# Kernel tuning notes

Hardware: AMD Instinct MI355X
Metric: run time of the kernel (lower is better)

## Reference

```python
import jax, jax.numpy as jnp
import numpy as np

N_EMBD = 1024
N_HEADS = 16
HEAD_EMBD = N_EMBD // N_HEADS  # 64
TOTAL = N_HEADS * HEAD_EMBD


def setup_inputs() -> dict:
    key = jax.random.key(0)
    k_x, k_wqkv, k_bqkv, k_wo, k_bo = jax.random.split(key, 5)
    B, S = 2, 2048
    x = jax.random.normal(k_x, (B, S, N_EMBD), dtype=jnp.float32)
    # torch nn.Linear: weight (out, in), y = x @ W.T + b
    lim_qkv = 1.0 / np.sqrt(N_EMBD)
    W_qkv = jax.random.uniform(k_wqkv, (3 * TOTAL, N_EMBD), minval=-lim_qkv, maxval=lim_qkv, dtype=jnp.float32)
    b_qkv = jax.random.uniform(k_bqkv, (3 * TOTAL,), minval=-lim_qkv, maxval=lim_qkv, dtype=jnp.float32)
    lim_o = 1.0 / np.sqrt(TOTAL)
    W_out = jax.random.uniform(k_wo, (N_EMBD, TOTAL), minval=-lim_o, maxval=lim_o, dtype=jnp.float32)
    b_out = jax.random.uniform(k_bo, (N_EMBD,), minval=-lim_o, maxval=lim_o, dtype=jnp.float32)
    return {"x": x, "W_qkv": W_qkv, "b_qkv": b_qkv, "W_out": W_out, "b_out": b_out}


def reference(x, W_qkv, b_qkv, W_out, b_out):
    B, S, _ = x.shape
    qkv = x @ W_qkv.T + b_qkv  # (B, S, 3*H*E)
    # rearrange 'b s (t h e) -> t b h s e'
    qkv = qkv.reshape(B, S, 3, N_HEADS, HEAD_EMBD)
    q = jnp.transpose(qkv[:, :, 0], (0, 2, 1, 3))  # (B, H, S, E)
    k = jnp.transpose(qkv[:, :, 1], (0, 2, 1, 3))
    v = jnp.transpose(qkv[:, :, 2], (0, 2, 1, 3))
    scores = jnp.einsum('bhse,bhte->bhst', q, k) / jnp.sqrt(jnp.float32(HEAD_EMBD))
    # original: tril(scores) + triu(-10000, k=1) == strict-upper entries exactly -10000
    row = jnp.arange(S)[:, None]
    col = jnp.arange(S)[None, :]
    masked = jnp.where(col > row, jnp.float32(-10000.0), scores)
    attn = jax.nn.softmax(masked, axis=-1)  # (B, H, S, S)
    z = jnp.einsum('bhrc,bhce->bhre', attn, v)  # (B, H, S, E)
    z = jnp.transpose(z, (0, 2, 1, 3)).reshape(B, S, TOTAL)
    out = z @ W_out.T + b_out
    return (out, attn)
```

## Files before the change

### kernel.cpp

```cpp
#include <hip/hip_runtime.h>
#include <stdint.h>

typedef __attribute__((ext_vector_type(4))) float f32x4;
typedef __attribute__((ext_vector_type(8))) short short8v;
typedef __attribute__((ext_vector_type(4))) unsigned short ushort4v;

#define DEV __device__ __forceinline__
#define EXP2 __builtin_amdgcn_exp2f
#define WAITVM0 asm volatile("s_waitcnt vmcnt(0)" ::: "memory")
#define WAITVM2 asm volatile("s_waitcnt vmcnt(2)" ::: "memory")
#define WAITVM4 asm volatile("s_waitcnt vmcnt(4)" ::: "memory")
#define FENCE   asm volatile("" ::: "memory")
#define BARRIER __builtin_amdgcn_s_barrier()

DEV unsigned short f2bf(float x) {
    union { float f; uint32_t u; } v; v.f = x;
    uint32_t r = v.u + 0x7fffu + ((v.u >> 16) & 1u);
    return (unsigned short)(r >> 16);
}
DEV float bf2f(unsigned short h) {
    union { uint32_t u; float f; } v; v.u = ((uint32_t)h) << 16;
    return v.f;
}
DEV uint32_t cvtpk(float lo, float hi) {
    uint32_t r;
    asm("v_cvt_pk_bf16_f32 %0, %1, %2" : "=v"(r) : "v"(lo), "v"(hi));
    return r;
}
DEV f32x4 mfma16(short8v a, short8v b, f32x4 c) {
    return __builtin_amdgcn_mfma_f32_16x16x32_bf16(a, b, c, 0, 0, 0);
}
DEV void gload16(const unsigned short* g, unsigned short* l) {
    __builtin_amdgcn_global_load_lds(
        (const __attribute__((address_space(1))) unsigned int*)g,
        (__attribute__((address_space(3))) unsigned int*)l, 16, 0, 0);
}
DEV void ntstore4(float* p, f32x4 v) { __builtin_nontemporal_store(v, (f32x4*)p); }

__global__ void k_cvt3(const float* __restrict__ a, unsigned short* __restrict__ oa, int na4,
                       const float* __restrict__ b, unsigned short* __restrict__ ob, int nb4,
                       const float* __restrict__ c, unsigned short* __restrict__ oc, int nc4) {
    int i = blockIdx.x * blockDim.x + threadIdx.x;
    const float* in; unsigned short* out; int idx;
    if (i < na4) { in = a; out = oa; idx = i; }
    else if (i < na4 + nb4) { in = b; out = ob; idx = i - na4; }
    else { idx = i - na4 - nb4; if (idx >= nc4) return; in = c; out = oc; }
    f32x4 v = *(const f32x4*)(in + (size_t)idx * 4);
    ushort4v h;
#pragma unroll
    for (int j = 0; j < 4; ++j) h[j] = f2bf(v[j]);
    *(ushort4v*)(out + (size_t)idx * 4) = h;
}

template <int KDIM>
DEV void gemm_core(const unsigned short* __restrict__ APTR,
                   const unsigned short* __restrict__ BPTR,
                   f32x4 (&acc)[4][4]) {
    __shared__ __align__(16) unsigned short As[2][128 * 32], Bs[2][128 * 32];
    int tid = threadIdx.x, lane = tid & 63, w = tid >> 6;
    int bm = blockIdx.x, bn = blockIdx.y;
    int wr = (w >> 1) * 64, wc = (w & 1) * 64;
    int lrow = lane & 15, lseg = lane >> 4;
#pragma unroll
    for (int m = 0; m < 4; ++m)
#pragma unroll
        for (int n = 0; n < 4; ++n) acc[m][n] = (f32x4){0.f, 0.f, 0.f, 0.f};
    auto STAGE = [&](int buf, int k0) {
#pragma unroll
        for (int i = 0; i < 2; ++i) {
            int ch = i * 256 + tid;
            int row = ch >> 2, seg = ch & 3;
            gload16(APTR + (size_t)(bm * 128 + row) * KDIM + k0 + seg * 8,
                    &As[buf][(i * 256 + (tid & ~63)) * 8]);
            gload16(BPTR + (size_t)(bn * 128 + row) * KDIM + k0 + seg * 8,
                    &Bs[buf][(i * 256 + (tid & ~63)) * 8]);
        }
    };
    const int NT = KDIM / 32;
    STAGE(0, 0);
    for (int t = 0; t < NT; ++t) {
        if (t < NT - 1) { STAGE((t + 1) & 1, (t + 1) * 32); WAITVM4; } else WAITVM0;
        BARRIER;
        const unsigned short* as = As[t & 1];
        const unsigned short* bs = Bs[t & 1];
        short8v fa[4], fb[4];
#pragma unroll
        for (int m = 0; m < 4; ++m) {
            fa[m] = *(const short8v*)(as + (wr + m * 16 + lrow) * 32 + lseg * 8);
            fb[m] = *(const short8v*)(bs + (wc + m * 16 + lrow) * 32 + lseg * 8);
        }
#pragma unroll
        for (int m = 0; m < 4; ++m)
#pragma unroll
            for (int n = 0; n < 4; ++n)
                acc[m][n] = mfma16(fa[m], fb[n], acc[m][n]);
        FENCE; BARRIER;
    }
}

__global__ __launch_bounds__(256) void k_gemm_qkv(
    const unsigned short* __restrict__ XB, const unsigned short* __restrict__ WB,
    const float* __restrict__ BIAS, unsigned short* __restrict__ QKVB) {
    f32x4 acc[4][4];
    gemm_core<1024>(XB, WB, acc);
    int tid = threadIdx.x, lane = tid & 63, w = tid >> 6;
    int bm = blockIdx.x, bn = blockIdx.y;
    int wr = (w >> 1) * 64, wc = (w & 1) * 64;
    int lrow = lane & 15, lseg = lane >> 4;
    const int N = 3072;
#pragma unroll
    for (int n = 0; n < 4; ++n) {
        int col = bn * 128 + wc + n * 16 + lrow;
        float bv = BIAS[col];
#pragma unroll
        for (int m = 0; m < 4; ++m) {
            int row = bm * 128 + wr + m * 16 + lseg * 4;
#pragma unroll
            for (int i = 0; i < 4; ++i)
                QKVB[(size_t)(row + i) * N + col] = f2bf(acc[m][n][i] + bv);
        }
    }
}

__global__ __launch_bounds__(256) void k_gemm_out(
    const unsigned short* __restrict__ ZB, const unsigned short* __restrict__ WOB,
    const float* __restrict__ BIAS, float* __restrict__ OUT) {
    f32x4 acc[4][4];
    gemm_core<1024>(ZB, WOB, acc);
    int tid = threadIdx.x, lane = tid & 63, w = tid >> 6;
    int bm = blockIdx.x, bn = blockIdx.y;
    int wr = (w >> 1) * 64, wc = (w & 1) * 64;
    int lrow = lane & 15, lseg = lane >> 4;
    const int N = 1024;
#pragma unroll
    for (int n = 0; n < 4; ++n) {
        int col = bn * 128 + wc + n * 16 + lrow;
        float bv = BIAS[col];
#pragma unroll
        for (int m = 0; m < 4; ++m) {
            int row = bm * 128 + wr + m * 16 + lseg * 4;
#pragma unroll
            for (int i = 0; i < 4; ++i)
                OUT[(size_t)(row + i) * N + col] = acc[m][n][i] + bv;
        }
    }
}

__global__ void k_prep_v(const unsigned short* __restrict__ QKVB, unsigned short* __restrict__ VT) {
    __shared__ unsigned short vt[32][72];
    int bh = blockIdx.y, b = bh >> 4, h = bh & 15;
    int c0 = blockIdx.x * 32;
    int t = threadIdx.x;
    int c = t >> 3, e8 = (t & 7) * 8;
    *(short8v*)&vt[c][e8] =
        *(const short8v*)(QKVB + (size_t)(b * 2048 + c0 + c) * 3072 + 2048 + h * 64 + e8);
    __syncthreads();
    int e = t & 63, cg = t >> 6;
    unsigned short tmp[8];
#pragma unroll
    for (int i = 0; i < 8; ++i) tmp[i] = vt[cg * 8 + i][e];
    *(short8v*)(VT + ((size_t)bh * 64 + e) * 2048 + c0 + cg * 8) = *(short8v*)tmp;
}

__global__ __launch_bounds__(512) void k_attn(
    const unsigned short* __restrict__ QKVB, const unsigned short* __restrict__ VT,
    float* __restrict__ ATTN, unsigned short* __restrict__ Z) {
    __shared__ __align__(16) unsigned short KV[2][8192];
    __shared__ __align__(16) float Pl[8][16][68];

    const float SCALE = 0.18033688011112042f;
    int blk = blockIdx.x;
    int bh = blk & 31;
    int rtp = blk >> 5;
    int rt = (rtp < 8) ? (15 - rtp) : (rtp - 8);
    int b = bh >> 4, h = bh & 15;
    int tid = threadIdx.x, lane = tid & 63, w = tid >> 6;
    int lrow = lane & 15, lseg = lane >> 4;
    int r0 = rt * 128 + w * 16;
    int T = 2 * rt + 2;
    int Tw = (r0 >> 6) + 1;

    short8v qf[2];
    {
        const unsigned short* qp =
            QKVB + (size_t)(b * 2048 + r0 + lrow) * 3072 + h * 64 + lseg * 8;
#pragma unroll
        for (int kc = 0; kc < 2; ++kc) {
            short8v qr = *(const short8v*)(qp + kc * 32);
            short8v qs;
#pragma unroll
            for (int j = 0; j < 8; ++j)
                qs[j] = (short)f2bf(bf2f((unsigned short)qr[j]) * SCALE);
            qf[kc] = qs;
        }
    }

    auto STAGEKA = [&](int buf, int t) {
        const size_t kbase = ((size_t)b * 2048 + (size_t)t * 128) * 3072 + 1024 + h * 64;
#pragma unroll
        for (int i2 = 0; i2 < 2; ++i2) {
            int ch = i2 * 512 + tid;
            int c = ch >> 3, u = ch & 7, us = u ^ (c & 7);
            gload16(QKVB + kbase + (size_t)c * 3072 + us * 8,
                    &KV[buf][(i2 * 512 + (tid & ~63)) * 8]);
        }
    };
    float ls4[4] = {0.f, 0.f, 0.f, 0.f};
    int TA = rt + 1;
    STAGEKA(0, 0);
    for (int t = 0; t < TA; ++t) {
        if (t < TA - 1) { STAGEKA((t + 1) & 1, t + 1); WAITVM2; } else WAITVM0;
        BARRIER;
        const unsigned short* kb = KV[t & 1];
        f32x4 sc[8];
#pragma unroll
        for (int g = 0; g < 8; ++g) sc[g] = (f32x4){0.f, 0.f, 0.f, 0.f};
#pragma unroll
        for (int kc = 0; kc < 2; ++kc) {
            int uoff = (((kc * 4 + lseg) ^ (lrow & 7)) << 3);
#pragma unroll
            for (int g = 0; g < 8; ++g) {
                short8v kf = *(const short8v*)(kb + (g * 16 + lrow) * 64 + uoff);
                sc[g] = mfma16(qf[kc], kf, sc[g]);
            }
        }
        if (t < TA - 1) {
#pragma unroll
            for (int g = 0; g < 8; ++g)
#pragma unroll
                for (int i = 0; i < 4; ++i) ls4[i] += EXP2(sc[g][i]);
        } else {
            int c0 = t * 128;
#pragma unroll
            for (int g = 0; g < 8; ++g)
#pragma unroll
                for (int i = 0; i < 4; ++i) {
                    float sv = (c0 + g * 16 + lrow > r0 + lseg * 4 + i) ? -1e30f : sc[g][i];
                    ls4[i] += EXP2(sv);
                }
        }
        FENCE; BARRIER;
    }
#pragma unroll
    for (int off = 1; off < 16; off <<= 1)
#pragma unroll
        for (int i = 0; i < 4; ++i) ls4[i] += __shfl_xor(ls4[i], off, 64);
    float invl[4];
#pragma unroll
    for (int i = 0; i < 4; ++i) invl[i] = 1.0f / ls4[i];

    auto STAGEKB = [&](int buf, int t) {
        const size_t kbase = ((size_t)b * 2048 + (size_t)t * 64) * 3072 + 1024 + h * 64;
        int c = tid >> 3, u = tid & 7, us = u ^ (c & 7);
        gload16(QKVB + kbase + (size_t)c * 3072 + us * 8, &KV[buf][(tid & ~63) * 8]);
    };
    auto STAGEVB = [&](int buf, int t) {
        const size_t vbase = (size_t)bh * 64 * 2048 + (size_t)t * 64;
        int e = tid >> 3, u = tid & 7, us = u ^ (e & 7);
        gload16(VT + vbase + (size_t)e * 2048 + us * 8, &KV[buf][4096 + (tid & ~63) * 8]);
    };

    float* ab = ATTN + ((size_t)bh * 2048 + r0) * 2048;
    f32x4 zacc[4];
#pragma unroll
    for (int i = 0; i < 4; ++i) zacc[i] = (f32x4){0.f, 0.f, 0.f, 0.f};

    STAGEKB(0, 0); STAGEVB(0, 0);
    for (int t = 0; t < T; ++t) {
        if (t < T - 1) { STAGEKB((t + 1) & 1, t + 1); STAGEVB((t + 1) & 1, t + 1); WAITVM2; }
        else WAITVM0;
        BARRIER;
        if (t < Tw) {
            const unsigned short* kb = KV[t & 1];
            const unsigned short* vb = KV[t & 1] + 4096;
            int c0 = t * 64;
            f32x4 sc[4];
#pragma unroll
            for (int g = 0; g < 4; ++g) sc[g] = (f32x4){0.f, 0.f, 0.f, 0.f};
#pragma unroll
            for (int kc = 0; kc < 2; ++kc) {
                int uoff = (((kc * 4 + lseg) ^ (lrow & 7)) << 3);
#pragma unroll
                for (int g = 0; g < 4; ++g) {
                    short8v kf = *(const short8v*)(kb + (g * 16 + lrow) * 64 + uoff);
                    sc[g] = mfma16(qf[kc], kf, sc[g]);
                }
            }
            if (t < Tw - 1) {
#pragma unroll
                for (int g = 0; g < 4; ++g)
#pragma unroll
                    for (int i = 0; i < 4; ++i)
                        Pl[w][lseg * 4 + i][g * 16 + lrow] = EXP2(sc[g][i]) * invl[i];
            } else {
#pragma unroll
                for (int g = 0; g < 4; ++g)
#pragma unroll
                    for (int i = 0; i < 4; ++i) {
                        float sv = (c0 + g * 16 + lrow > r0 + lseg * 4 + i) ? -1e30f : sc[g][i];
                        Pl[w][lseg * 4 + i][g * 16 + lrow] = EXP2(sv) * invl[i];
                    }
            }
            short8v pf[2];
#pragma unroll
            for (int kc = 0; kc < 2; ++kc) {
                f32x4 p0 = *(const f32x4*)&Pl[w][lrow][kc * 32 + lseg * 8];
                f32x4 p1 = *(const f32x4*)&Pl[w][lrow][kc * 32 + lseg * 8 + 4];
                union { uint32_t u[4]; short8v s; } pu;
                pu.u[0] = cvtpk(p0[0], p0[1]);
                pu.u[1] = cvtpk(p0[2], p0[3]);
                pu.u[2] = cvtpk(p1[0], p1[1]);
                pu.u[3] = cvtpk(p1[2], p1[3]);
                pf[kc] = pu.s;
            }
#pragma unroll
            for (int kc = 0; kc < 2; ++kc) {
                int uoff = (((kc * 4 + lseg) ^ (lrow & 7)) << 3);
#pragma unroll
                for (int et = 0; et < 4; ++et) {
                    short8v vf = *(const short8v*)(vb + (et * 16 + lrow) * 64 + uoff);
                    zacc[et] = mfma16(pf[kc], vf, zacc[et]);
                }
            }
            {
                int row4 = lane >> 4, cq = lane & 15;
#pragma unroll
                for (int r4 = 0; r4 < 4; ++r4) {
                    int row = r4 * 4 + row4;
                    ntstore4(ab + (size_t)row * 2048 + c0 + cq * 4,
                             *(const f32x4*)(&Pl[w][row][cq * 4]));
                }
            }
        }
        FENCE; BARRIER;
    }

#pragma unroll
    for (int et = 0; et < 4; ++et)
#pragma unroll
        for (int i = 0; i < 4; ++i)
            Z[(size_t)(b * 2048 + r0 + lseg * 4 + i) * 1024 + h * 64 + et * 16 + lrow] =
                f2bf(zacc[et][i]);

    int czw = Tw * 64;
    const f32x4 zz = (f32x4){0.f, 0.f, 0.f, 0.f};
    for (int r = 0; r < 16; ++r) {
        float* rp = ab + (size_t)r * 2048;
        for (int c = czw + (lane << 2); c < 2048; c += 256)
            ntstore4(rp + c, zz);
    }
}

extern "C" void kernel_launch(void* const* d_in, const int* in_sizes, int n_in,
                              void* d_out, int out_size, void* d_ws, size_t ws_size,
                              hipStream_t stream) {
    const float* X    = (const float*)d_in[0];
    const float* Wqkv = (const float*)d_in[1];
    const float* Bqkv = (const float*)d_in[2];
    const float* Wout = (const float*)d_in[3];
    const float* Bout = (const float*)d_in[4];
    float* out  = (float*)d_out;
    float* attn = out + (size_t)4096 * 1024;

    char* ws = (char*)d_ws;
    unsigned short* QKVB = (unsigned short*)ws; ws += (size_t)4096 * 3072 * 2;
    unsigned short* VTp  = (unsigned short*)ws; ws += (size_t)32 * 64 * 2048 * 2;
    unsigned short* ZBp  = (unsigned short*)ws; ws += (size_t)4096 * 1024 * 2;
    unsigned short* XBp  = (unsigned short*)ws; ws += (size_t)4096 * 1024 * 2;
    unsigned short* WQBp = (unsigned short*)ws; ws += (size_t)3072 * 1024 * 2;
    unsigned short* WOBp = (unsigned short*)ws; ws += (size_t)1024 * 1024 * 2;

    const int na4 = 4096 * 1024 / 4, nb4 = 3072 * 1024 / 4, nc4 = 1024 * 1024 / 4;
    k_cvt3<<<(na4 + nb4 + nc4 + 255) / 256, 256, 0, stream>>>(
        X, XBp, na4, Wqkv, WQBp, nb4, Wout, WOBp, nc4);
    k_gemm_qkv<<<dim3(32, 24), 256, 0, stream>>>(XBp, WQBp, Bqkv, QKVB);
    k_prep_v<<<dim3(64, 32), 256, 0, stream>>>(QKVB, VTp);
    k_attn<<<512, 512, 0, stream>>>(QKVB, VTp, attn, ZBp);
    k_gemm_out<<<dim3(32, 8), 256, 0, stream>>>(ZBp, WOBp, Bout, out);
}
```

Baseline: 230.1 us.

## Split attention into row-sum kernel and PV kernel, move zero-fill earlier

Splits the attention kernel in two. The first kernel computes the softmax row sums, writes their inverses to a workspace buffer, and zero-fills the masked upper triangle of the attention matrix. The second kernel reads the inverse sums and does the probability write-out and PV accumulation. This shortens each kernel's critical path and shifts the zero-fill stores off the PV kernel. It costs an extra launch and an extra Rinv buffer, and the Q loads are repeated across both kernels. It also switches the output GEMM stores to nontemporal stores.

```diff
diff --git a/kernel.cpp b/kernel.cpp
--- a/kernel.cpp
+++ b/kernel.cpp
@@ -141,7 +141,8 @@
             int row = bm * 128 + wr + m * 16 + lseg * 4;
 #pragma unroll
             for (int i = 0; i < 4; ++i)
-                OUT[(size_t)(row + i) * N + col] = acc[m][n][i] + bv;
+                __builtin_nontemporal_store(acc[m][n][i] + bv,
+                                            OUT + (size_t)(row + i) * N + col);
         }
     }
 }
@@ -162,9 +163,106 @@
     *(short8v*)(VT + ((size_t)bh * 64 + e) * 2048 + c0 + cg * 8) = *(short8v*)tmp;
 }
 
-__global__ __launch_bounds__(512) void k_attn(
+__global__ __launch_bounds__(512) void k_attn_sums(
+    const unsigned short* __restrict__ QKVB, float* __restrict__ Rinv,
+    float* __restrict__ ATTN) {
+    __shared__ __align__(16) unsigned short Kt[2][8192];
+
+    const float SCALE = 0.18033688011112042f;
+    int blk = blockIdx.x;
+    int bh = blk & 31;
+    int rtp = blk >> 5;
+    int rt = (rtp < 8) ? (15 - rtp) : (rtp - 8);
+    int b = bh >> 4, h = bh & 15;
+    int tid = threadIdx.x, lane = tid & 63, w = tid >> 6;
+    int lrow = lane & 15, lseg = lane >> 4;
+    int r0 = rt * 128 + w * 16;
+    int TA = rt + 1;
+
+    short8v qf[2];
+    {
+        const unsigned short* qp =
+            QKVB + (size_t)(b * 2048 + r0 + lrow) * 3072 + h * 64 + lseg * 8;
+#pragma unroll
+        for (int kc = 0; kc < 2; ++kc) {
+            short8v qr = *(const short8v*)(qp + kc * 32);
+            short8v qs;
+#pragma unroll
+            for (int j = 0; j < 8; ++j)
+                qs[j] = (short)f2bf(bf2f((unsigned short)qr[j]) * SCALE);
+            qf[kc] = qs;
+        }
+    }
+
+    auto STAGEKA = [&](int buf, int t) {
+        const size_t kbase = ((size_t)b * 2048 + (size_t)t * 128) * 3072 + 1024 + h * 64;
+#pragma unroll
+        for (int i2 = 0; i2 < 2; ++i2) {
+            int ch = i2 * 512 + tid;
+            int c = ch >> 3, u = ch & 7, us = u ^ (c & 7);
+            gload16(QKVB + kbase + (size_t)c * 3072 + us * 8,
+                    &Kt[buf][(i2 * 512 + (tid & ~63)) * 8]);
+        }
+    };
+    float ls4[4] = {0.f, 0.f, 0.f, 0.f};
+    STAGEKA(0, 0);
+    for (int t = 0; t < TA; ++t) {
+        if (t < TA - 1) { STAGEKA((t + 1) & 1, t + 1); WAITVM2; } else WAITVM0;
+        BARRIER;
+        const unsigned short* kb = Kt[t & 1];
+        f32x4 sc[8];
+#pragma unroll
+        for (int g = 0; g < 8; ++g) sc[g] = (f32x4){0.f, 0.f, 0.f, 0.f};
+#pragma unroll
+        for (int kc = 0; kc < 2; ++kc) {
+            int uoff = (((kc * 4 + lseg) ^ (lrow & 7)) << 3);
+#pragma unroll
+            for (int g = 0; g < 8; ++g) {
+                short8v kf = *(const short8v*)(kb + (g * 16 + lrow) * 64 + uoff);
+                sc[g] = mfma16(qf[kc], kf, sc[g]);
+            }
+        }
+        if (t < TA - 1) {
+#pragma unroll
+            for (int g = 0; g < 8; ++g)
+#pragma unroll
+                for (int i = 0; i < 4; ++i) ls4[i] += EXP2(sc[g][i]);
+        } else {
+            int c0 = t * 128;
+#pragma unroll
+            for (int g = 0; g < 8; ++g)
+#pragma unroll
+                for (int i = 0; i < 4; ++i) {
+                    float sv = (c0 + g * 16 + lrow > r0 + lseg * 4 + i) ? -1e30f : sc[g][i];
+                    ls4[i] += EXP2(sv);
+                }
+        }
+        FENCE; BARRIER;
+    }
+#pragma unroll
+    for (int off = 1; off < 16; off <<= 1)
+#pragma unroll
+        for (int i = 0; i < 4; ++i) ls4[i] += __shfl_xor(ls4[i], off, 64);
+    if (lrow == 0) {
+#pragma unroll
+        for (int i = 0; i < 4; ++i)
+            Rinv[(size_t)bh * 2048 + r0 + lseg * 4 + i] = 1.0f / ls4[i];
+    }
+
+    float* ab = ATTN + ((size_t)bh * 2048 + r0) * 2048;
+    int czw = ((r0 >> 6) + 1) * 64;
+    const f32x4 zz = (f32x4){0.f, 0.f, 0.f, 0.f};
+    for (int r = 0; r < 16; ++r) {
+        float* rp = ab + (size_t)r * 2048;
+        for (int c = czw + (lane << 2); c < 2048; c += 256)
+            ntstore4(rp + c, zz);
+    }
+}
+
+__global__ __launch_bounds__(512) void k_attn_pv(
     const unsigned short* __restrict__ QKVB, const unsigned short* __restrict__ VT,
-    float* __restrict__ ATTN, unsigned short* __restrict__ Z) {
+    const float* __restrict__ Rinv, float* __restrict__ ATTN,
+    unsigned short* __restrict__ Z) {
     __shared__ __align__(16) unsigned short KV[2][8192];
     __shared__ __align__(16) float Pl[8][16][68];
 
@@ -194,60 +292,12 @@
             qf[kc] = qs;
         }
     }
-
-    auto STAGEKA = [&](int buf, int t) {
-        const size_t kbase = ((size_t)b * 2048 + (size_t)t * 128) * 3072 + 1024 + h * 64;
-#pragma unroll
-        for (int i2 = 0; i2 < 2; ++i2) {
-            int ch = i2 * 512 + tid;
-            int c = ch >> 3, u = ch & 7, us = u ^ (c & 7);
-            gload16(QKVB + kbase + (size_t)c * 3072 + us * 8,
-                    &KV[buf][(i2 * 512 + (tid & ~63)) * 8]);
-        }
-    };
-    float ls4[4] = {0.f, 0.f, 0.f, 0.f};
-    int TA = rt + 1;
-    STAGEKA(0, 0);
-    for (int t = 0; t < TA; ++t) {
-        if (t < TA - 1) { STAGEKA((t + 1) & 1, t + 1); WAITVM2; } else WAITVM0;
-        BARRIER;
-        const unsigned short* kb = KV[t & 1];
-        f32x4 sc[8];
-#pragma unroll
-        for (int g = 0; g < 8; ++g) sc[g] = (f32x4){0.f, 0.f, 0.f, 0.f};
-#pragma unroll
-        for (int kc = 0; kc < 2; ++kc) {
-            int uoff = (((kc * 4 + lseg) ^ (lrow & 7)) << 3);
-#pragma unroll
-            for (int g = 0; g < 8; ++g) {
-                short8v kf = *(const short8v*)(kb + (g * 16 + lrow) * 64 + uoff);
-                sc[g] = mfma16(qf[kc], kf, sc[g]);
-            }
-        }
-        if (t < TA - 1) {
-#pragma unroll
-            for (int g = 0; g < 8; ++g)
-#pragma unroll
-                for (int i = 0; i < 4; ++i) ls4[i] += EXP2(sc[g][i]);
-        } else {
-            int c0 = t * 128;
-#pragma unroll
-            for (int g = 0; g < 8; ++g)
-#pragma unroll
-                for (int i = 0; i < 4; ++i) {
-                    float sv = (c0 + g * 16 + lrow > r0 + lseg * 4 + i) ? -1e30f : sc[g][i];
-                    ls4[i] += EXP2(sv);
-                }
-        }
-        FENCE; BARRIER;
-    }
-#pragma unroll
-    for (int off = 1; off < 16; off <<= 1)
-#pragma unroll
-        for (int i = 0; i < 4; ++i) ls4[i] += __shfl_xor(ls4[i], off, 64);
     float invl[4];
-#pragma unroll
-    for (int i = 0; i < 4; ++i) invl[i] = 1.0f / ls4[i];
+    {
+        f32x4 iv = *(const f32x4*)(Rinv + (size_t)bh * 2048 + r0 + lseg * 4);
+#pragma unroll
+        for (int i = 0; i < 4; ++i) invl[i] = iv[i];
+    }
 
     auto STAGEKB = [&](int buf, int t) {
         const size_t kbase = ((size_t)b * 2048 + (size_t)t * 64) * 3072 + 1024 + h * 64;
@@ -341,14 +391,6 @@
         for (int i = 0; i < 4; ++i)
             Z[(size_t)(b * 2048 + r0 + lseg * 4 + i) * 1024 + h * 64 + et * 16 + lrow] =
                 f2bf(zacc[et][i]);
-
-    int czw = Tw * 64;
-    const f32x4 zz = (f32x4){0.f, 0.f, 0.f, 0.f};
-    for (int r = 0; r < 16; ++r) {
-        float* rp = ab + (size_t)r * 2048;
-        for (int c = czw + (lane << 2); c < 2048; c += 256)
-            ntstore4(rp + c, zz);
-    }
 }
 
 extern "C" void kernel_launch(void* const* d_in, const int* in_sizes, int n_in,
@@ -369,12 +411,14 @@
     unsigned short* XBp  = (unsigned short*)ws; ws += (size_t)4096 * 1024 * 2;
     unsigned short* WQBp = (unsigned short*)ws; ws += (size_t)3072 * 1024 * 2;
     unsigned short* WOBp = (unsigned short*)ws; ws += (size_t)1024 * 1024 * 2;
+    float* RinvP         = (float*)ws;          ws += (size_t)32 * 2048 * 4;
 
     const int na4 = 4096 * 1024 / 4, nb4 = 3072 * 1024 / 4, nc4 = 1024 * 1024 / 4;
     k_cvt3<<<(na4 + nb4 + nc4 + 255) / 256, 256, 0, stream>>>(
         X, XBp, na4, Wqkv, WQBp, nb4, Wout, WOBp, nc4);
     k_gemm_qkv<<<dim3(32, 24), 256, 0, stream>>>(XBp, WQBp, Bqkv, QKVB);
     k_prep_v<<<dim3(64, 32), 256, 0, stream>>>(QKVB, VTp);
-    k_attn<<<512, 512, 0, stream>>>(QKVB, VTp, attn, ZBp);
+    k_attn_sums<<<512, 512, 0, stream>>>(QKVB, RinvP, attn);
+    k_attn_pv<<<512, 512, 0, stream>>>(QKVB, VTp, RinvP, attn, ZBp);
     k_gemm_out<<<dim3(32, 8), 256, 0, stream>>>(ZBp, WOBp, Bout, out);
 }
```

Result: slower. 246.7 us (+7.2%).
